# Kernel optimization log

Measured on AMD Instinct MI355X. Metric: run time of the kernel, lower is better.

## Reference

```python
import jax, jax.numpy as jnp
import numpy as np

P = 8        # patch size
STRIDE = 4   # reference patch stride
SR = 12      # search radius
SS = 3       # search step -> 9x9 = 81 candidates
K = 16       # group size (3rd dim of 3D transform)
LAM = 2.7    # hard threshold multiplier
TWO_STEP = True


def _dct_mat(n):
    k = np.arange(n)[:, None].astype(np.float64)
    i = np.arange(n)[None, :].astype(np.float64)
    m = np.cos(np.pi * (2 * i + 1) * k / (2 * n)) * np.sqrt(2.0 / n)
    m[0] /= np.sqrt(2.0)
    return jnp.asarray(m, jnp.float32)


def _hadamard(n):
    h = np.array([[1.0]])
    while h.shape[0] < n:
        h = np.kron(h, np.array([[1.0, 1.0], [1.0, -1.0]])) / np.sqrt(2.0)
    return jnp.asarray(h, jnp.float32)

D8 = _dct_mat(P)
H16 = _hadamard(K)


def _extract_patches(img):
    # img (H, W) -> (Hp*Wp, P*P) patches at stride 1
    H, W = img.shape
    Hp, Wp = H - P + 1, W - P + 1
    cols = [img[di:di + Hp, dj:dj + Wp] for di in range(P) for dj in range(P)]
    return jnp.stack(cols, -1).reshape(Hp * Wp, P * P), Hp, Wp


def _block_match(patches, Hp, Wp):
    # returns (N, K) flat patch indices of best-matching groups
    ri = jnp.arange(0, Hp, STRIDE)
    rj = jnp.arange(0, Wp, STRIDE)
    RI, RJ = jnp.meshgrid(ri, rj, indexing='ij')
    RI, RJ = RI.reshape(-1), RJ.reshape(-1)                     # (N,)
    offs = jnp.arange(-SR, SR + 1, SS)
    OI, OJ = jnp.meshgrid(offs, offs, indexing='ij')
    ci = jnp.clip(RI[:, None] + OI.reshape(-1)[None, :], 0, Hp - 1)
    cj = jnp.clip(RJ[:, None] + OJ.reshape(-1)[None, :], 0, Wp - 1)
    cidx = ci * Wp + cj                                         # (N, C)
    cand = patches[cidx]                                        # (N, C, 64)
    ref = patches[RI * Wp + RJ]                                 # (N, 64)
    dist = (jnp.sum(cand * cand, -1)
            - 2.0 * jnp.einsum('nce,ne->nc', cand, ref)
            + jnp.sum(ref * ref, -1)[:, None])
    _, top = jax.lax.top_k(-dist, K)
    return jnp.take_along_axis(cidx, top, axis=1)               # (N, K)


def _fwd3d(groups):
    # (N, K, P*P) -> 3D transform coeffs (N, K, P, P)
    g = groups.reshape(groups.shape[0], K, P, P)
    c = jnp.einsum('ab,nkbc,dc->nkad', D8, g, D8)   # 2D DCT per patch
    return jnp.einsum('gk,nkad->ngad', H16, c)      # 1D Hadamard across group


def _inv3d(coef):
    c = jnp.einsum('gk,ngad->nkad', H16, coef)      # H^T (orthonormal)
    g = jnp.einsum('ab,nkad,dc->nkbc', D8, c, D8)   # inverse 2D DCT
    return g.reshape(coef.shape[0], K, P * P)


def _aggregate(vals, w, gidx, Hp, Wp, H, W):
    # vals (N,K,64) filtered patches, w (N,) group weights, gidx (N,K)
    gi, gj = gidx // Wp, gidx % Wp
    offs = (jnp.arange(P)[:, None] * W + jnp.arange(P)[None, :]).reshape(-1)
    pix = ((gi * W + gj)[..., None] + offs).reshape(-1)         # (N*K*64,)
    wv = jnp.broadcast_to(w[:, None, None], vals.shape)
    num = jnp.zeros(H * W, jnp.float32).at[pix].add((wv * vals).reshape(-1))
    den = jnp.zeros(H * W, jnp.float32).at[pix].add(wv.reshape(-1))
    return (num / jnp.maximum(den, 1e-8)).reshape(H, W)


def _bm3d_channel(img, sigma2):
    H, W = img.shape
    sigma2 = jnp.float32(sigma2)
    sigma = jnp.sqrt(sigma2)
    patches, Hp, Wp = _extract_patches(img)

    # ---- step 1: hard-threshold collaborative filtering ----
    gidx = _block_match(patches, Hp, Wp)
    groups = patches[gidx]                                      # (N,K,64)
    coef = _fwd3d(groups)
    mask = (jnp.abs(coef) > LAM * sigma)
    mask = mask.at[:, 0, 0, 0].set(True)                        # keep DC
    coef_ht = jnp.where(mask, coef, 0.0)
    nnz = jnp.sum(mask.astype(jnp.float32), axis=(1, 2, 3))
    w_ht = 1.0 / (sigma2 * jnp.maximum(nnz, 1.0))
    basic = _aggregate(_inv3d(coef_ht), w_ht, gidx, Hp, Wp, H, W)
    if not TWO_STEP:
        return basic

    # ---- step 2: Wiener filtering using the basic estimate ----
    patches_b, _, _ = _extract_patches(basic)
    gidx2 = _block_match(patches_b, Hp, Wp)
    cb = _fwd3d(patches_b[gidx2])                               # basic coeffs
    cn = _fwd3d(patches[gidx2])                                 # noisy coeffs
    wien = cb * cb / (cb * cb + sigma2)
    coef_w = wien * cn
    w_wie = 1.0 / (sigma2 * jnp.maximum(jnp.sum(wien * wien, axis=(1, 2, 3)), 1e-8))
    return _aggregate(_inv3d(coef_w), w_wie, gidx2, Hp, Wp, H, W)


def setup_inputs() -> dict:
    key = jax.random.key(0)
    im = jax.random.randint(key, (1, 1, 384, 384), 0, 256, dtype=jnp.int32)
    return {"im": im, "variance": 25}


def reference(im, variance):
    # im: (1, 1, H, W) int tensor, values >= 0; variance: scalar noise variance
    outs = [_bm3d_channel(im[0, c].astype(jnp.float32), variance)
            for c in range(im.shape[1])]
    return jnp.stack(outs, 0)[None]                             # (1, C, H, W) float32
```

## Files before the change

kernel.cpp:

```cpp
#include <hip/hip_runtime.h>
#include <math.h>

#define TS 45
#define FINF 3.4e38f

__device__ __forceinline__ int iclip(int v, int hi) {
  return v < 0 ? 0 : (v > hi ? hi : v);
}

constexpr float CA = 0.35355339059327373f;
constexpr float K1 = 0.49039264020161522f;
constexpr float K2 = 0.46193976625564337f;
constexpr float K3 = 0.41573480615127262f;
constexpr float K4 = 0.35355339059327379f;
constexpr float K5 = 0.27778511650980111f;
constexpr float K6 = 0.19134171618254489f;
constexpr float K7 = 0.097545161008064135f;

constexpr float DCT8[8][8] = {
  { CA, CA, CA, CA, CA, CA, CA, CA},
  { K1, K3, K5, K7,-K7,-K5,-K3,-K1},
  { K2, K6,-K6,-K2,-K2,-K6, K6, K2},
  { K3,-K7,-K1,-K5, K5, K1, K7,-K3},
  { K4,-K4,-K4, K4, K4,-K4,-K4, K4},
  { K5,-K1, K7, K3,-K3,-K7, K1,-K5},
  { K6,-K2, K2,-K6,-K6, K2,-K2, K6},
  { K7,-K5, K3,-K1, K1,-K3, K5,-K7},
};

__device__ __forceinline__ int sxor_i(int v, int m) {
  switch (m) {
    case 1:  return __builtin_amdgcn_update_dpp(0, v, 0xB1, 0xF, 0xF, true);
    case 2:  return __builtin_amdgcn_update_dpp(0, v, 0x4E, 0xF, 0xF, true);
    case 4:  return __builtin_amdgcn_ds_swizzle(v, (4 << 10) | 0x1F);
    case 8:  return __builtin_amdgcn_ds_swizzle(v, (8 << 10) | 0x1F);
    case 16: return __builtin_amdgcn_ds_swizzle(v, (16 << 10) | 0x1F);
    default: return __shfl_xor(v, 32, 64);
  }
}
__device__ __forceinline__ float sxor_f(float v, int m) {
  return __int_as_float(sxor_i(__float_as_int(v), m));
}

__device__ __forceinline__ float qbcast(float v, int s) {
  int x = __float_as_int(v), r;
  switch (s) {
    case 0:  r = __builtin_amdgcn_update_dpp(0, x, 0x00, 0xF, 0xF, true); break;
    case 1:  r = __builtin_amdgcn_update_dpp(0, x, 0x55, 0xF, 0xF, true); break;
    case 2:  r = __builtin_amdgcn_update_dpp(0, x, 0xAA, 0xF, 0xF, true); break;
    default: r = __builtin_amdgcn_update_dpp(0, x, 0xFF, 0xF, 0xF, true); break;
  }
  return __int_as_float(r);
}

__device__ __forceinline__ void fwd_rowcol(float X[2][8], float U[2][8],
                                           const float Ca0[8], const float Ca1[8]) {
#pragma unroll
  for (int r = 0; r < 2; r++)
#pragma unroll
    for (int d = 0; d < 8; d++) {
      float s = X[r][0] * DCT8[d][0];
#pragma unroll
      for (int c = 1; c < 8; c++) s += X[r][c] * DCT8[d][c];
      U[r][d] = s;
    }
#pragma unroll
  for (int r = 0; r < 2; r++)
#pragma unroll
    for (int d = 0; d < 8; d++) X[r][d] = 0.f;
#pragma unroll
  for (int b = 0; b < 8; b++)
#pragma unroll
    for (int d = 0; d < 8; d++) {
      float yb = qbcast(U[b & 1][d], b >> 1);
      X[0][d] += Ca0[b] * yb;
      X[1][d] += Ca1[b] * yb;
    }
}

__device__ __forceinline__ void inv_colrow(float X[2][8], float U[2][8],
                                           const float Ct0[8], const float Ct1[8]) {
#pragma unroll
  for (int r = 0; r < 2; r++)
#pragma unroll
    for (int d = 0; d < 8; d++) U[r][d] = 0.f;
#pragma unroll
  for (int a = 0; a < 8; a++)
#pragma unroll
    for (int d = 0; d < 8; d++) {
      float za = qbcast(X[a & 1][d], a >> 1);
      U[0][d] += Ct0[a] * za;
      U[1][d] += Ct1[a] * za;
    }
#pragma unroll
  for (int r = 0; r < 2; r++)
#pragma unroll
    for (int c = 0; c < 8; c++) {
      float s = U[r][0] * DCT8[0][c];
#pragma unroll
      for (int d = 1; d < 8; d++) s += U[r][d] * DCT8[d][c];
      X[r][c] = s;
    }
}

__device__ __forceinline__ void had16r(float X[2][8], int lane) {
#pragma unroll
  for (int m = 4; m <= 32; m <<= 1) {
    bool hi = (lane & m) != 0;
#pragma unroll
    for (int r = 0; r < 2; r++)
#pragma unroll
      for (int d = 0; d < 8; d++) {
        float tv = sxor_f(X[r][d], m);
        X[r][d] = hi ? (tv - X[r][d]) : (X[r][d] + tv);
      }
  }
#pragma unroll
  for (int r = 0; r < 2; r++)
#pragma unroll
    for (int d = 0; d < 8; d++) X[r][d] *= 0.25f;
}

template <int WIEN>
__device__ __forceinline__ void group_worker(
    const float* __restrict__ tileS, const float* __restrict__ tileN,
    float* __restrict__ accN, float* __restrict__ accD,
    const float* __restrict__ ldsD, int* __restrict__ sel,
    int lane, int ri, int rj, int bi, int ub, float sigma2) {

  int cB = lane < 17 ? 64 + lane : 80;
  int aiA = iclip(ri + (lane / 9) * 3 - 12, 376) - bi;
  int ajA = iclip(rj + (lane % 9) * 3 - 12, 376) - ub;
  int aiB = iclip(ri + (cB / 9) * 3 - 12, 376) - bi;
  int ajB = iclip(rj + (cB % 9) * 3 - 12, 376) - ub;
  int roi = ri - bi, roj = rj - ub;
  float sccA = 0.f, scrA = 0.f, sccB = 0.f, scrB = 0.f, srr = 0.f;
#pragma unroll
  for (int i = 0; i < 8; i++) {
    const float* rr = tileS + (roi + i) * TS + roj;
    const float* ar = tileS + (aiA + i) * TS + ajA;
    const float* br = tileS + (aiB + i) * TS + ajB;
#pragma unroll
    for (int j = 0; j < 8; j++) {
      float rv = rr[j], av = ar[j], bv = br[j];
      sccA += av * av; scrA += av * rv;
      sccB += bv * bv; scrB += bv * rv;
      srr  += rv * rv;
    }
  }
  float d0 = sccA - 2.f * scrA + srr; int i0 = lane;
  float d1 = lane < 17 ? (sccB - 2.f * scrB + srr) : FINF; int i1 = 64 + lane;

#pragma unroll 1
  for (int r = 0; r < 16; r++) {
    float d = d0; int i = i0;
    if (d1 < d0) { d = d1; i = i1; }
#pragma unroll
    for (int m = 1; m <= 32; m <<= 1) {
      float dd = sxor_f(d, m); int ii = sxor_i(i, m);
      if (dd < d || (dd == d && ii < i)) { d = dd; i = ii; }
    }
    if (lane == 0) {
      int si = iclip(ri + (i / 9) * 3 - 12, 376) - bi;
      int sj = iclip(rj + (i % 9) * 3 - 12, 376) - ub;
      sel[r] = (si << 8) | sj;
    }
    if (i == i0) d0 = FINF;
    if (i == i1) d1 = FINF;
  }

  int q = lane & 3, k = lane >> 2;
  float Ca0[8], Ca1[8];
#pragma unroll
  for (int b = 0; b < 8; b++) {
    Ca0[b] = ldsD[(2 * q) * 8 + b];
    Ca1[b] = ldsD[(2 * q + 1) * 8 + b];
  }
  int sp = sel[k];
  int gi = (sp >> 8) + 2 * q, gj = sp & 255;

  float X[2][8], U[2][8], ZB[2][8];
  float w;

  if (WIEN) {
#pragma unroll
    for (int r = 0; r < 2; r++)
#pragma unroll
      for (int c = 0; c < 8; c++) ZB[r][c] = tileS[(gi + r) * TS + gj + c];
    fwd_rowcol(ZB, U, Ca0, Ca1);
    had16r(ZB, lane);
  }

#pragma unroll
  for (int r = 0; r < 2; r++)
#pragma unroll
    for (int c = 0; c < 8; c++) X[r][c] = tileN[(gi + r) * TS + gj + c];
  fwd_rowcol(X, U, Ca0, Ca1);
  had16r(X, lane);

  if (WIEN) {
    float part = 0.f;
#pragma unroll
    for (int r = 0; r < 2; r++)
#pragma unroll
      for (int d = 0; d < 8; d++) {
        float cb = ZB[r][d];
        float we = cb * cb / (cb * cb + sigma2);
        X[r][d] = we * X[r][d];
        part += we * we;
      }
#pragma unroll
    for (int m = 1; m <= 32; m <<= 1) part += sxor_f(part, m);
    w = 1.f / (sigma2 * fmaxf(part, 1e-8f));
  } else {
    float thr = 2.7f * sqrtf(sigma2);
    int cnt = 0;
#pragma unroll
    for (int r = 0; r < 2; r++)
#pragma unroll
      for (int d = 0; d < 8; d++) {
        bool keep = (fabsf(X[r][d]) > thr) || (lane == 0 && r == 0 && d == 0);
        cnt += (int)__popcll(__ballot(keep));
        if (!keep) X[r][d] = 0.f;
      }
    w = 1.f / (sigma2 * fmaxf((float)cnt, 1.f));
  }

  had16r(X, lane);
#pragma unroll
  for (int a = 0; a < 8; a++) {
    Ca0[a] = ldsD[a * 8 + 2 * q];
    Ca1[a] = ldsD[a * 8 + 2 * q + 1];
  }
  inv_colrow(X, U, Ca0, Ca1);

#pragma unroll
  for (int r = 0; r < 2; r++)
#pragma unroll
    for (int c = 0; c < 8; c++) {
      int off = (gi + r) * TS + gj + c;
      atomicAdd(&accN[off], w * X[r][c]);
      atomicAdd(&accD[off], w);
    }
}

template <int WIEN>
__global__ __launch_bounds__(256, 5) void bm3d_pass(
    const int* __restrict__ img, const float* __restrict__ basic,
    const int* __restrict__ pvar,
    float* __restrict__ num, float* __restrict__ den) {
  __shared__ float ldsD[64];
  __shared__ int   ldsSel[4][16];
  __shared__ float tileN[32 * TS];
  __shared__ float tileB[WIEN ? 32 * TS : 1];
  __shared__ float accN[32 * TS], accD[32 * TS];

  int t = threadIdx.x;
  int brow = blockIdx.x / 24, bcb = blockIdx.x - brow * 24;
  int ri = brow * 4;
  int bim = ri - 12;      int bi = bim < 0 ? 0 : (bim > 352 ? 352 : bim);
  int ubm = 16 * bcb - 12; int ub = ubm < 0 ? 0 : (ubm > 352 ? 352 : ubm);

  if (t < 64) ldsD[t] = DCT8[t >> 3][t & 7];
  for (int e = t; e < 32 * 44; e += 256) {
    int r = e / 44, c = e - r * 44;
    int col = ub + c;
    bool ok = col < 384;
    tileN[r * TS + c] = ok ? (float)img[(bi + r) * 384 + col] : 0.f;
    if (WIEN) tileB[r * TS + c] = ok ? basic[(bi + r) * 384 + col] : 0.f;
  }
  for (int e = t; e < 32 * TS; e += 256) { accN[e] = 0.f; accD[e] = 0.f; }
  __syncthreads();

  float sigma2 = (float)pvar[0];
  int wv = t >> 6, lane = t & 63;
  int gc = bcb * 4 + wv;
  if (gc < 95) {
    group_worker<WIEN>(WIEN ? tileB : tileN, tileN, accN, accD, ldsD,
                       &ldsSel[wv][0], lane, ri, gc * 4, bi, ub, sigma2);
  }
  __syncthreads();

  for (int e = t; e < 32 * TS; e += 256) {
    float dv = accD[e];
    if (dv != 0.f) {
      int r = e / TS, c = e - r * TS;
      int gp = (bi + r) * 384 + ub + c;
      atomicAdd(&num[gp], accN[e]);
      atomicAdd(&den[gp], dv);
    }
  }
}

__global__ void div_kernel(const float* __restrict__ num,
                           const float* __restrict__ den,
                           float* __restrict__ out, int npix) {
  int i = blockIdx.x * blockDim.x + threadIdx.x;
  if (i < npix) out[i] = num[i] / fmaxf(den[i], 1e-8f);
}

extern "C" void kernel_launch(void* const* d_in, const int* in_sizes, int n_in,
                              void* d_out, int out_size, void* d_ws, size_t ws_size,
                              hipStream_t stream) {
  const int* img  = (const int*)d_in[0];
  const int* pvar = (const int*)d_in[1];
  float* out = (float*)d_out;
  float* ws  = (float*)d_ws;

  const int NPIX = 384 * 384;
  float* num1  = ws + 0 * NPIX;
  float* den1  = ws + 1 * NPIX;
  float* basic = ws + 2 * NPIX;
  float* num2  = ws + 3 * NPIX;
  float* den2  = ws + 4 * NPIX;

  hipMemsetAsync(num1, 0, (size_t)2 * NPIX * sizeof(float), stream);
  hipMemsetAsync(num2, 0, (size_t)2 * NPIX * sizeof(float), stream);

  const int NBLK = 95 * 24;
  bm3d_pass<0><<<NBLK, 256, 0, stream>>>(img, nullptr, pvar, num1, den1);
  div_kernel<<<(NPIX + 255) / 256, 256, 0, stream>>>(num1, den1, basic, NPIX);
  bm3d_pass<1><<<NBLK, 256, 0, stream>>>(img, basic, pvar, num2, den2);
  div_kernel<<<(NPIX + 255) / 256, 256, 0, stream>>>(num2, den2, out, NPIX);
}
```

Measured before the change: 297.2 us.

## Alias LDS tiles with accumulators, vectorize tile load, raise occupancy

The separate accumulator arrays are removed. The two image-tile buffers are reused as numerator and denominator accumulators once the transforms are finished, with an extra barrier and zeroing pass between the two uses. This cuts LDS per block so the launch bound goes from 5 to 8 blocks per CU. The tile load now uses int4/float4 vector loads with TS=44, and the per-wave selection array in LDS is replaced by each lane keeping its own chosen match in registers. The cost is holding the transform results in registers across the barriers, plus possible LDS bank conflicts now that the row stride is 44.

```diff
diff --git a/kernel.cpp b/kernel.cpp
--- a/kernel.cpp
+++ b/kernel.cpp
@@ -1,7 +1,7 @@
 #include <hip/hip_runtime.h>
 #include <math.h>
 
-#define TS 45
+#define TS 44
 #define FINF 3.4e38f
 
 __device__ __forceinline__ int iclip(int v, int hi) {
@@ -122,171 +122,193 @@
 }
 
 template <int WIEN>
-__device__ __forceinline__ void group_worker(
-    const float* __restrict__ tileS, const float* __restrict__ tileN,
-    float* __restrict__ accN, float* __restrict__ accD,
-    const float* __restrict__ ldsD, int* __restrict__ sel,
-    int lane, int ri, int rj, int bi, int ub, float sigma2) {
-
-  int cB = lane < 17 ? 64 + lane : 80;
-  int aiA = iclip(ri + (lane / 9) * 3 - 12, 376) - bi;
-  int ajA = iclip(rj + (lane % 9) * 3 - 12, 376) - ub;
-  int aiB = iclip(ri + (cB / 9) * 3 - 12, 376) - bi;
-  int ajB = iclip(rj + (cB % 9) * 3 - 12, 376) - ub;
-  int roi = ri - bi, roj = rj - ub;
-  float sccA = 0.f, scrA = 0.f, sccB = 0.f, scrB = 0.f, srr = 0.f;
-#pragma unroll
-  for (int i = 0; i < 8; i++) {
-    const float* rr = tileS + (roi + i) * TS + roj;
-    const float* ar = tileS + (aiA + i) * TS + ajA;
-    const float* br = tileS + (aiB + i) * TS + ajB;
-#pragma unroll
-    for (int j = 0; j < 8; j++) {
-      float rv = rr[j], av = ar[j], bv = br[j];
-      sccA += av * av; scrA += av * rv;
-      sccB += bv * bv; scrB += bv * rv;
-      srr  += rv * rv;
-    }
-  }
-  float d0 = sccA - 2.f * scrA + srr; int i0 = lane;
-  float d1 = lane < 17 ? (sccB - 2.f * scrB + srr) : FINF; int i1 = 64 + lane;
-
-#pragma unroll 1
-  for (int r = 0; r < 16; r++) {
-    float d = d0; int i = i0;
-    if (d1 < d0) { d = d1; i = i1; }
-#pragma unroll
-    for (int m = 1; m <= 32; m <<= 1) {
-      float dd = sxor_f(d, m); int ii = sxor_i(i, m);
-      if (dd < d || (dd == d && ii < i)) { d = dd; i = ii; }
-    }
-    if (lane == 0) {
-      int si = iclip(ri + (i / 9) * 3 - 12, 376) - bi;
-      int sj = iclip(rj + (i % 9) * 3 - 12, 376) - ub;
-      sel[r] = (si << 8) | sj;
-    }
-    if (i == i0) d0 = FINF;
-    if (i == i1) d1 = FINF;
-  }
-
-  int q = lane & 3, k = lane >> 2;
-  float Ca0[8], Ca1[8];
-#pragma unroll
-  for (int b = 0; b < 8; b++) {
-    Ca0[b] = ldsD[(2 * q) * 8 + b];
-    Ca1[b] = ldsD[(2 * q + 1) * 8 + b];
-  }
-  int sp = sel[k];
-  int gi = (sp >> 8) + 2 * q, gj = sp & 255;
-
-  float X[2][8], U[2][8], ZB[2][8];
-  float w;
-
-  if (WIEN) {
-#pragma unroll
-    for (int r = 0; r < 2; r++)
-#pragma unroll
-      for (int c = 0; c < 8; c++) ZB[r][c] = tileS[(gi + r) * TS + gj + c];
-    fwd_rowcol(ZB, U, Ca0, Ca1);
-    had16r(ZB, lane);
-  }
-
-#pragma unroll
-  for (int r = 0; r < 2; r++)
-#pragma unroll
-    for (int c = 0; c < 8; c++) X[r][c] = tileN[(gi + r) * TS + gj + c];
-  fwd_rowcol(X, U, Ca0, Ca1);
-  had16r(X, lane);
-
-  if (WIEN) {
-    float part = 0.f;
-#pragma unroll
-    for (int r = 0; r < 2; r++)
-#pragma unroll
-      for (int d = 0; d < 8; d++) {
-        float cb = ZB[r][d];
-        float we = cb * cb / (cb * cb + sigma2);
-        X[r][d] = we * X[r][d];
-        part += we * we;
-      }
-#pragma unroll
-    for (int m = 1; m <= 32; m <<= 1) part += sxor_f(part, m);
-    w = 1.f / (sigma2 * fmaxf(part, 1e-8f));
-  } else {
-    float thr = 2.7f * sqrtf(sigma2);
-    int cnt = 0;
-#pragma unroll
-    for (int r = 0; r < 2; r++)
-#pragma unroll
-      for (int d = 0; d < 8; d++) {
-        bool keep = (fabsf(X[r][d]) > thr) || (lane == 0 && r == 0 && d == 0);
-        cnt += (int)__popcll(__ballot(keep));
-        if (!keep) X[r][d] = 0.f;
-      }
-    w = 1.f / (sigma2 * fmaxf((float)cnt, 1.f));
-  }
-
-  had16r(X, lane);
-#pragma unroll
-  for (int a = 0; a < 8; a++) {
-    Ca0[a] = ldsD[a * 8 + 2 * q];
-    Ca1[a] = ldsD[a * 8 + 2 * q + 1];
-  }
-  inv_colrow(X, U, Ca0, Ca1);
-
-#pragma unroll
-  for (int r = 0; r < 2; r++)
-#pragma unroll
-    for (int c = 0; c < 8; c++) {
-      int off = (gi + r) * TS + gj + c;
-      atomicAdd(&accN[off], w * X[r][c]);
-      atomicAdd(&accD[off], w);
-    }
-}
-
-template <int WIEN>
-__global__ __launch_bounds__(256, 5) void bm3d_pass(
+__global__ __launch_bounds__(256, 8) void bm3d_pass(
     const int* __restrict__ img, const float* __restrict__ basic,
     const int* __restrict__ pvar,
     float* __restrict__ num, float* __restrict__ den) {
   __shared__ float ldsD[64];
-  __shared__ int   ldsSel[4][16];
-  __shared__ float tileN[32 * TS];
-  __shared__ float tileB[WIEN ? 32 * TS : 1];
-  __shared__ float accN[32 * TS], accD[32 * TS];
+  __shared__ float bufA[32 * TS];
+  __shared__ float bufB[32 * TS];
 
   int t = threadIdx.x;
   int brow = blockIdx.x / 24, bcb = blockIdx.x - brow * 24;
   int ri = brow * 4;
-  int bim = ri - 12;      int bi = bim < 0 ? 0 : (bim > 352 ? 352 : bim);
+  int bim = ri - 12;       int bi = bim < 0 ? 0 : (bim > 352 ? 352 : bim);
   int ubm = 16 * bcb - 12; int ub = ubm < 0 ? 0 : (ubm > 352 ? 352 : ubm);
 
   if (t < 64) ldsD[t] = DCT8[t >> 3][t & 7];
-  for (int e = t; e < 32 * 44; e += 256) {
-    int r = e / 44, c = e - r * 44;
-    int col = ub + c;
-    bool ok = col < 384;
-    tileN[r * TS + c] = ok ? (float)img[(bi + r) * 384 + col] : 0.f;
-    if (WIEN) tileB[r * TS + c] = ok ? basic[(bi + r) * 384 + col] : 0.f;
-  }
-  for (int e = t; e < 32 * TS; e += 256) { accN[e] = 0.f; accD[e] = 0.f; }
+
+  for (int e4 = t; e4 < 32 * 11; e4 += 256) {
+    int r = e4 / 11, c4 = (e4 - r * 11) << 2;
+    int col = ub + c4;
+    int gidx = (bi + r) * 384 + col;
+    int o = r * TS + c4;
+    if (col + 3 < 384) {
+      int4 iv = *(const int4*)&img[gidx];
+      float4 fv = make_float4((float)iv.x, (float)iv.y, (float)iv.z, (float)iv.w);
+      if (WIEN) {
+        *(float4*)&bufA[o] = *(const float4*)&basic[gidx];
+        *(float4*)&bufB[o] = fv;
+      } else {
+        *(float4*)&bufA[o] = fv;
+      }
+    } else {
+#pragma unroll
+      for (int u = 0; u < 4; u++) {
+        bool ok = (col + u) < 384;
+        float fi = ok ? (float)img[gidx + u] : 0.f;
+        if (WIEN) {
+          bufA[o + u] = ok ? basic[gidx + u] : 0.f;
+          bufB[o + u] = fi;
+        } else {
+          bufA[o + u] = fi;
+        }
+      }
+    }
+  }
   __syncthreads();
 
   float sigma2 = (float)pvar[0];
   int wv = t >> 6, lane = t & 63;
   int gc = bcb * 4 + wv;
-  if (gc < 95) {
-    group_worker<WIEN>(WIEN ? tileB : tileN, tileN, accN, accD, ldsD,
-                       &ldsSel[wv][0], lane, ri, gc * 4, bi, ub, sigma2);
-  }
+  bool active = gc < 95;
+
+  float X[2][8];
+  float w = 0.f;
+  int gi0 = 0, gj0 = 0;
+
+  if (active) {
+    int rj = gc * 4;
+    const float* tileS = bufA;
+    const float* tileN = WIEN ? bufB : bufA;
+
+    int cB = lane < 17 ? 64 + lane : 80;
+    int aiA = iclip(ri + (lane / 9) * 3 - 12, 376) - bi;
+    int ajA = iclip(rj + (lane % 9) * 3 - 12, 376) - ub;
+    int aiB = iclip(ri + (cB / 9) * 3 - 12, 376) - bi;
+    int ajB = iclip(rj + (cB % 9) * 3 - 12, 376) - ub;
+    int roi = ri - bi, roj = rj - ub;
+    float sccA = 0.f, scrA = 0.f, sccB = 0.f, scrB = 0.f, srr = 0.f;
+#pragma unroll
+    for (int i = 0; i < 8; i++) {
+      const float* rr = tileS + (roi + i) * TS + roj;
+      const float* ar = tileS + (aiA + i) * TS + ajA;
+      const float* br = tileS + (aiB + i) * TS + ajB;
+#pragma unroll
+      for (int j = 0; j < 8; j++) {
+        float rv = rr[j], av = ar[j], bv = br[j];
+        sccA += av * av; scrA += av * rv;
+        sccB += bv * bv; scrB += bv * rv;
+        srr  += rv * rv;
+      }
+    }
+    float d0 = sccA - 2.f * scrA + srr; int i0 = lane;
+    float d1 = lane < 17 ? (sccB - 2.f * scrB + srr) : FINF; int i1 = 64 + lane;
+
+    int k = lane >> 2, q = lane & 3;
+    int msi = 0, msj = 0;
+#pragma unroll 1
+    for (int r = 0; r < 16; r++) {
+      float d = d0; int i = i0;
+      if (d1 < d0) { d = d1; i = i1; }
+#pragma unroll
+      for (int m = 1; m <= 32; m <<= 1) {
+        float dd = sxor_f(d, m); int ii = sxor_i(i, m);
+        if (dd < d || (dd == d && ii < i)) { d = dd; i = ii; }
+      }
+      if (r == k) {
+        msi = iclip(ri + (i / 9) * 3 - 12, 376) - bi;
+        msj = iclip(rj + (i % 9) * 3 - 12, 376) - ub;
+      }
+      if (i == i0) d0 = FINF;
+      if (i == i1) d1 = FINF;
+    }
+
+    float Ca0[8], Ca1[8];
+#pragma unroll
+    for (int b = 0; b < 8; b++) {
+      Ca0[b] = ldsD[(2 * q) * 8 + b];
+      Ca1[b] = ldsD[(2 * q + 1) * 8 + b];
+    }
+    gi0 = msi + 2 * q; gj0 = msj;
+
+    float U[2][8], ZB[2][8];
+
+    if (WIEN) {
+#pragma unroll
+      for (int r = 0; r < 2; r++)
+#pragma unroll
+        for (int c = 0; c < 8; c++) ZB[r][c] = tileS[(gi0 + r) * TS + gj0 + c];
+      fwd_rowcol(ZB, U, Ca0, Ca1);
+      had16r(ZB, lane);
+    }
+
+#pragma unroll
+    for (int r = 0; r < 2; r++)
+#pragma unroll
+      for (int c = 0; c < 8; c++) X[r][c] = tileN[(gi0 + r) * TS + gj0 + c];
+    fwd_rowcol(X, U, Ca0, Ca1);
+    had16r(X, lane);
+
+    if (WIEN) {
+      float part = 0.f;
+#pragma unroll
+      for (int r = 0; r < 2; r++)
+#pragma unroll
+        for (int d = 0; d < 8; d++) {
+          float cb = ZB[r][d];
+          float we = cb * cb / (cb * cb + sigma2);
+          X[r][d] = we * X[r][d];
+          part += we * we;
+        }
+#pragma unroll
+      for (int m = 1; m <= 32; m <<= 1) part += sxor_f(part, m);
+      w = 1.f / (sigma2 * fmaxf(part, 1e-8f));
+    } else {
+      float thr = 2.7f * sqrtf(sigma2);
+      int cnt = 0;
+#pragma unroll
+      for (int r = 0; r < 2; r++)
+#pragma unroll
+        for (int d = 0; d < 8; d++) {
+          bool keep = (fabsf(X[r][d]) > thr) || (lane == 0 && r == 0 && d == 0);
+          cnt += (int)__popcll(__ballot(keep));
+          if (!keep) X[r][d] = 0.f;
+        }
+      w = 1.f / (sigma2 * fmaxf((float)cnt, 1.f));
+    }
+
+    had16r(X, lane);
+#pragma unroll
+    for (int a = 0; a < 8; a++) {
+      Ca0[a] = ldsD[a * 8 + 2 * q];
+      Ca1[a] = ldsD[a * 8 + 2 * q + 1];
+    }
+    inv_colrow(X, U, Ca0, Ca1);
+  }
+
   __syncthreads();
+  for (int e = t; e < 32 * TS; e += 256) { bufA[e] = 0.f; bufB[e] = 0.f; }
+  __syncthreads();
+
+  if (active) {
+#pragma unroll
+    for (int r = 0; r < 2; r++)
+#pragma unroll
+      for (int c = 0; c < 8; c++) {
+        int off = (gi0 + r) * TS + gj0 + c;
+        atomicAdd(&bufA[off], w * X[r][c]);
+        atomicAdd(&bufB[off], w);
+      }
+  }
+  __syncthreads();
 
   for (int e = t; e < 32 * TS; e += 256) {
-    float dv = accD[e];
+    float dv = bufB[e];
     if (dv != 0.f) {
       int r = e / TS, c = e - r * TS;
       int gp = (bi + r) * 384 + ub + c;
-      atomicAdd(&num[gp], accN[e]);
+      atomicAdd(&num[gp], bufA[e]);
       atomicAdd(&den[gp], dv);
     }
   }
```

After: 307.8 us. 1.04x slower.
